# Kernel tuning notes

Measured on AMD Instinct MI355X. Metric: run time of the kernel, lower is better.

The kernel has to match this reference:

```python
import jax, jax.numpy as jnp
import numpy as np

EPS = 1e-6

def _layernorm(x, gamma, beta):
    # normalize over last dim (head_dim)
    mean = x.mean(axis=-1, keepdims=True)
    var = x.var(axis=-1, keepdims=True)
    return gamma * (x - mean) * jax.lax.rsqrt(var + EPS) + beta

def setup_inputs() -> dict:
    key = jax.random.key(0)
    ks = jax.random.split(key, 6)
    B, N, C, H = 2, 2048, 1024, 16
    Dh = C // H
    x = jax.random.normal(ks[0], (B, N, C), dtype=jnp.float32)
    qkv_w = jax.random.normal(ks[1], (C, 3 * C), dtype=jnp.float32) * (1.0 / np.sqrt(C))
    q_gamma = jnp.ones((Dh,), jnp.float32)
    q_beta = jnp.zeros((Dh,), jnp.float32)
    k_gamma = jnp.ones((Dh,), jnp.float32)
    k_beta = jnp.zeros((Dh,), jnp.float32)
    proj_w = jax.random.normal(ks[2], (C, C), dtype=jnp.float32) * (1.0 / np.sqrt(C))
    proj_b = jnp.zeros((C,), jnp.float32)
    return {"x": x, "qkv_w": qkv_w, "q_gamma": q_gamma, "q_beta": q_beta,
            "k_gamma": k_gamma, "k_beta": k_beta, "proj_w": proj_w, "proj_b": proj_b}

def reference(x, qkv_w, q_gamma, q_beta, k_gamma, k_beta, proj_w, proj_b):
    B, N, C = x.shape
    H = 16
    Dh = C // H
    scale = Dh ** -0.5
    qkv = x @ qkv_w                                   # [B,N,3C]
    qkv = qkv.reshape(B, N, 3, H, Dh)
    q = qkv[:, :, 0].transpose(0, 2, 1, 3)            # [B,H,N,Dh]
    k = qkv[:, :, 1].transpose(0, 2, 1, 3)
    v = qkv[:, :, 2].transpose(0, 2, 1, 3)
    q = _layernorm(q, q_gamma, q_beta)
    k = _layernorm(k, k_gamma, k_beta)
    attn = jnp.einsum('bhnd,bhmd->bhnm', q, k) * scale
    attn = jax.nn.softmax(attn, axis=-1)
    out = jnp.einsum('bhnm,bhmd->bhnd', attn, v)      # [B,H,N,Dh]
    out = out.transpose(0, 2, 1, 3).reshape(B, N, C)
    return out @ proj_w + proj_b
```

## Files before the change

### kernel.cpp

```cpp
#include <hip/hip_runtime.h>

typedef unsigned short u16;
typedef unsigned int u32;
typedef float f32x4 __attribute__((ext_vector_type(4)));
typedef float f32x16 __attribute__((ext_vector_type(16)));
typedef short s16x8 __attribute__((ext_vector_type(8)));

#define B_ 2
#define N_ 2048
#define C_ 1024
#define H_ 16
#define BN_ (B_*N_)

#define EXP2F(x) __builtin_amdgcn_exp2f(x)

__device__ __forceinline__ u16 f2bf(float f) {
  union { float f; unsigned u; } c; c.f = f;
  unsigned u = c.u;
  u = (u + 0x7fffu + ((u >> 16) & 1u)) >> 16;
  return (u16)u;
}
__device__ __forceinline__ float bf2f(u16 h) {
  union { unsigned u; float f; } c; c.u = ((unsigned)h) << 16;
  return c.f;
}
__device__ __forceinline__ u32 pack2(float lo, float hi) {
  u32 r;
  asm("v_cvt_pk_bf16_f32 %0, %1, %2" : "=v"(r) : "v"(lo), "v"(hi));
  return r;
}
__device__ __forceinline__ void plswap(u32& a, u32& b) {
  asm volatile("v_permlane32_swap_b32 %0, %1" : "+v"(a), "+v"(b));
}
__device__ __forceinline__ void gload16(const u16* g, u16* l) {
  __builtin_amdgcn_global_load_lds(
      (const __attribute__((address_space(1))) unsigned*)g,
      (__attribute__((address_space(3))) unsigned*)l, 16, 0, 0);
}

__global__ __launch_bounds__(256) void k_cast_bf16(const float* __restrict__ x,
                                                   u16* __restrict__ o, int n4) {
  int i = blockIdx.x * blockDim.x + threadIdx.x;
  if (i >= n4) return;
  float4 v = ((const float4*)x)[i];
  ushort4 r;
  r.x = f2bf(v.x); r.y = f2bf(v.y); r.z = f2bf(v.z); r.w = f2bf(v.w);
  ((ushort4*)o)[i] = r;
}

__global__ __launch_bounds__(256) void k_transpose_cast(const float* __restrict__ W,
                                                        u16* __restrict__ Wt,
                                                        int R, int Cc) {
  __shared__ float t[32][33];
  int tx = threadIdx.x, ty = threadIdx.y;
  int c0 = blockIdx.x * 32, r0 = blockIdx.y * 32;
#pragma unroll
  for (int i = 0; i < 4; ++i)
    t[ty + i * 8][tx] = W[(long)(r0 + ty + i * 8) * Cc + c0 + tx];
  __syncthreads();
#pragma unroll
  for (int i = 0; i < 4; ++i)
    Wt[(long)(c0 + ty + i * 8) * R + r0 + tx] = f2bf(t[tx][ty + i * 8]);
}

__global__ __launch_bounds__(256) void k_gemm_qkv_ln(const u16* __restrict__ A,
                                                     const u16* __restrict__ Bt,
                                                     const float* __restrict__ qg,
                                                     const float* __restrict__ qbeta,
                                                     const float* __restrict__ kg,
                                                     const float* __restrict__ kbeta,
                                                     u16* __restrict__ Qh,
                                                     u16* __restrict__ Kh,
                                                     u16* __restrict__ Vt) {
  const int K = C_;
  __shared__ u16 smem[32768];
  int tid = threadIdx.x;
  int w = tid >> 6, l = tid & 63;
  int l15 = l & 15, lhi = l >> 4;
  int wm = w >> 1, wn = w & 1;
  int rowA = l >> 3;
  int colA = ((l & 7) ^ (rowA & 7)) * 8;
  int x0 = (lhi ^ (l15 & 7)) * 8;
  int x1 = ((4 + lhi) ^ (l15 & 7)) * 8;
  const u16* Ab = A + (long)blockIdx.y * 128 * K;
  const u16* Bb = Bt + (long)blockIdx.x * 128 * K;
  f32x4 acc[4][4];
#pragma unroll
  for (int m = 0; m < 4; ++m)
#pragma unroll
    for (int n = 0; n < 4; ++n)
      acc[m][n] = (f32x4){0.f, 0.f, 0.f, 0.f};

  auto STAGE = [&](int k0, int bi) {
    u16* at = smem + bi * 8192;
    u16* bt = smem + 16384 + bi * 8192;
#pragma unroll
    for (int i = 0; i < 4; ++i) {
      int ci = i * 4 + w;
      gload16(Ab + (long)(ci * 8 + rowA) * K + k0 + colA, &at[ci * 512]);
      gload16(Bb + (long)(ci * 8 + rowA) * K + k0 + colA, &bt[ci * 512]);
    }
  };

  const int NS = K / 64;
  STAGE(0, 0);
  for (int t = 0; t < NS; ++t) {
    __builtin_amdgcn_s_barrier();
    if (t + 1 < NS) {
      STAGE((t + 1) * 64, (t + 1) & 1);
      asm volatile("s_waitcnt vmcnt(8)" ::: "memory");
    } else {
      asm volatile("s_waitcnt vmcnt(0)" ::: "memory");
    }
    __builtin_amdgcn_s_barrier();
    const u16* at = smem + (t & 1) * 8192;
    const u16* bt = smem + 16384 + (t & 1) * 8192;
#pragma unroll
    for (int kk = 0; kk < 2; ++kk) {
      int xo = kk ? x1 : x0;
      s16x8 af[4], bfr[4];
#pragma unroll
      for (int m = 0; m < 4; ++m)
        af[m] = *(const s16x8*)&at[(wm * 64 + m * 16 + l15) * 64 + xo];
#pragma unroll
      for (int n = 0; n < 4; ++n)
        bfr[n] = *(const s16x8*)&bt[(wn * 64 + n * 16 + l15) * 64 + xo];
#pragma unroll
      for (int m = 0; m < 4; ++m)
#pragma unroll
        for (int n = 0; n < 4; ++n)
          acc[m][n] = __builtin_amdgcn_mfma_f32_16x16x32_bf16(af[m], bfr[n], acc[m][n], 0, 0, 0);
    }
  }

  int cb = blockIdx.x * 128 + wn * 64;
  int s = cb >> 10;
  int h = (cb & 1023) >> 6;
  int rowbase = blockIdx.y * 128 + wm * 64;

  if (s == 2) {
    __syncthreads();
    u16* tbuf = smem + w * 4608;
    u32* tb32 = (u32*)tbuf;
#pragma unroll
    for (int m = 0; m < 4; ++m)
#pragma unroll
      for (int n = 0; n < 4; ++n) {
        int d = n * 16 + l15;
#pragma unroll
        for (int r = 0; r < 4; r += 2)
          tb32[d * 36 + m * 8 + lhi * 2 + (r >> 1)] =
              pack2(acc[m][n][r], acc[m][n][r + 1]);
      }
    int b = rowbase >> 11;
    int nnb = rowbase & (N_ - 1);
    int bhv = b * H_ + h;
    int ch = (l & 7) * 8;
#pragma unroll
    for (int i = 0; i < 8; ++i) {
      int dl = i * 8 + (l >> 3);
      s16x8 vv = *(const s16x8*)&tbuf[dl * 72 + ch];
      *(s16x8*)&Vt[(long)(bhv * 64 + dl) * N_ + nnb + ch] = vv;
    }
  } else {
    const float* g = (s == 0) ? qg : kg;
    const float* be = (s == 0) ? qbeta : kbeta;
    u16* Oh = (s == 0) ? Qh : Kh;
    float sc = (s == 0) ? 0.125f * 1.44269504089f : 1.f;
    float gv[4], bv[4];
#pragma unroll
    for (int n = 0; n < 4; ++n) { gv[n] = g[n * 16 + l15]; bv[n] = be[n * 16 + l15]; }
#pragma unroll
    for (int m = 0; m < 4; ++m) {
#pragma unroll
      for (int r = 0; r < 4; ++r) {
        float t = (acc[m][0][r] + acc[m][1][r]) + (acc[m][2][r] + acc[m][3][r]);
        t += __shfl_xor(t, 1); t += __shfl_xor(t, 2);
        t += __shfl_xor(t, 4); t += __shfl_xor(t, 8);
        float mean = t * (1.f / 64.f);
        float v0 = acc[m][0][r] - mean, v1 = acc[m][1][r] - mean;
        float v2 = acc[m][2][r] - mean, v3 = acc[m][3][r] - mean;
        float q2 = (v0 * v0 + v1 * v1) + (v2 * v2 + v3 * v3);
        q2 += __shfl_xor(q2, 1); q2 += __shfl_xor(q2, 2);
        q2 += __shfl_xor(q2, 4); q2 += __shfl_xor(q2, 8);
        float rs = rsqrtf(q2 * (1.f / 64.f) + 1e-6f);
        int row = rowbase + m * 16 + lhi * 4 + r;
        int b = row >> 11, nn = row & (N_ - 1);
        long ob = ((long)(b * H_ + h) * N_ + nn) * 64;
        float vv[4] = {v0, v1, v2, v3};
#pragma unroll
        for (int n = 0; n < 4; ++n)
          Oh[ob + n * 16 + l15] = f2bf(sc * (gv[n] * vv[n] * rs + bv[n]));
      }
    }
  }
}

__global__ __launch_bounds__(256) void k_gemm_proj(const u16* __restrict__ A,
                                                   const u16* __restrict__ Bt,
                                                   float* __restrict__ Cout,
                                                   const float* __restrict__ bias,
                                                   int M, int N, int K) {
  __shared__ u16 a_t[2][128 * 64];
  __shared__ u16 b_t[2][128 * 64];
  int tid = threadIdx.x;
  int w = tid >> 6, l = tid & 63;
  int l15 = l & 15, lhi = l >> 4;
  int wm = w >> 1, wn = w & 1;
  int rowA = l >> 3;
  int colA = ((l & 7) ^ (rowA & 7)) * 8;
  int x0 = (lhi ^ (l15 & 7)) * 8;
  int x1 = ((4 + lhi) ^ (l15 & 7)) * 8;
  const u16* Ab = A + (long)blockIdx.y * 128 * K;
  const u16* Bb = Bt + (long)blockIdx.x * 128 * K;
  f32x4 acc[4][4];
#pragma unroll
  for (int m = 0; m < 4; ++m)
#pragma unroll
    for (int n = 0; n < 4; ++n)
      acc[m][n] = (f32x4){0.f, 0.f, 0.f, 0.f};

  auto STAGE = [&](int k0, int bi) {
#pragma unroll
    for (int i = 0; i < 4; ++i) {
      int ci = i * 4 + w;
      gload16(Ab + (long)(ci * 8 + rowA) * K + k0 + colA, &a_t[bi][ci * 512]);
      gload16(Bb + (long)(ci * 8 + rowA) * K + k0 + colA, &b_t[bi][ci * 512]);
    }
  };

  const int NS = 1024 / 64;
  STAGE(0, 0);
  for (int t = 0; t < NS; ++t) {
    __builtin_amdgcn_s_barrier();
    if (t + 1 < NS) {
      STAGE((t + 1) * 64, (t + 1) & 1);
      asm volatile("s_waitcnt vmcnt(8)" ::: "memory");
    } else {
      asm volatile("s_waitcnt vmcnt(0)" ::: "memory");
    }
    __builtin_amdgcn_s_barrier();
    const u16* at = a_t[t & 1];
    const u16* bt = b_t[t & 1];
#pragma unroll
    for (int kk = 0; kk < 2; ++kk) {
      int xo = kk ? x1 : x0;
      s16x8 af[4], bfr[4];
#pragma unroll
      for (int m = 0; m < 4; ++m)
        af[m] = *(const s16x8*)&at[(wm * 64 + m * 16 + l15) * 64 + xo];
#pragma unroll
      for (int n = 0; n < 4; ++n)
        bfr[n] = *(const s16x8*)&bt[(wn * 64 + n * 16 + l15) * 64 + xo];
#pragma unroll
      for (int m = 0; m < 4; ++m)
#pragma unroll
        for (int n = 0; n < 4; ++n)
          acc[m][n] = __builtin_amdgcn_mfma_f32_16x16x32_bf16(af[m], bfr[n], acc[m][n], 0, 0, 0);
    }
  }
#pragma unroll
  for (int m = 0; m < 4; ++m) {
#pragma unroll
    for (int n = 0; n < 4; ++n) {
      int col = blockIdx.x * 128 + wn * 64 + n * 16 + l15;
#pragma unroll
      for (int r = 0; r < 4; ++r) {
        int row = blockIdx.y * 128 + wm * 64 + m * 16 + lhi * 4 + r;
        Cout[(long)row * N + col] = acc[m][n][r] + bias[col];
      }
    }
  }
}

__global__ __launch_bounds__(512, 4) void k_attn(const u16* __restrict__ Qh,
                                                 const u16* __restrict__ Kh,
                                                 const u16* __restrict__ Vt,
                                                 u16* __restrict__ O) {
  __shared__ u16 k_t[2][2][64 * 64];
  __shared__ u16 v_t[2][2][64 * 64];
  int tid = threadIdx.x;
  int w = tid >> 6, l = tid & 63;
  int half = w >> 2, wq = w & 3;
  int l31 = l & 31, hi = l >> 5;
  int id = blockIdx.x;
  int swz = (id & 7) * 64 + (id >> 3);
  int bh = swz >> 4, qb = swz & 15;
  int b = bh >> 4, h = bh & 15;
  const u16* Qb = Qh + ((long)bh * N_ + qb * 128 + wq * 32) * 64;
  const u16* Kb = Kh + ((long)bh * N_ + half * 1024) * 64;
  const u16* Vb = Vt + (long)bh * 64 * N_ + half * 1024;

  s16x8 qf[4];
#pragma unroll
  for (int j = 0; j < 4; ++j)
    qf[j] = *(const s16x8*)&Qb[l31 * 64 + j * 16 + hi * 8];

  f32x16 acc0, acc1;
#pragma unroll
  for (int i = 0; i < 16; ++i) { acc0[i] = 0.f; acc1[i] = 0.f; }
  float lsum = 0.f;

  int off[2][4];
#pragma unroll
  for (int t = 0; t < 2; ++t)
#pragma unroll
    for (int j = 0; j < 4; ++j)
      off[t][j] = (t * 32 + l31) * 64 + (((j * 2 + hi) ^ (l & 7)) * 8);

  int srow = l >> 3;
  int scol = ((l & 7) ^ srow) * 8;

  auto STAGE = [&](int kt, int bi) {
#pragma unroll
    for (int i = 0; i < 2; ++i) {
      int ci = i * 4 + wq;
      gload16(Kb + (long)(kt + ci * 8 + srow) * 64 + scol, &k_t[half][bi][ci * 512]);
      gload16(Vb + (long)(ci * 8 + srow) * N_ + kt + scol, &v_t[half][bi][ci * 512]);
    }
  };

  const int NT = 16;
  STAGE(0, 0);

  for (int t = 0; t < NT; ++t) {
    __builtin_amdgcn_s_barrier();
    if (t + 1 < NT) {
      STAGE((t + 1) * 64, (t + 1) & 1);
      asm volatile("s_waitcnt vmcnt(4)" ::: "memory");
    } else {
      asm volatile("s_waitcnt vmcnt(0)" ::: "memory");
    }
    __builtin_amdgcn_s_barrier();
    const u16* kb = k_t[half][t & 1];
    const u16* vb = v_t[half][t & 1];

    f32x16 s0, s1;
#pragma unroll
    for (int i = 0; i < 16; ++i) { s0[i] = 0.f; s1[i] = 0.f; }
    __builtin_amdgcn_s_setprio(1);
#pragma unroll
    for (int j = 0; j < 4; ++j) {
      s16x8 kf0 = *(const s16x8*)&kb[off[0][j]];
      s0 = __builtin_amdgcn_mfma_f32_32x32x16_bf16(kf0, qf[j], s0, 0, 0, 0);
      s16x8 kf1 = *(const s16x8*)&kb[off[1][j]];
      s1 = __builtin_amdgcn_mfma_f32_32x32x16_bf16(kf1, qf[j], s1, 0, 0, 0);
    }
    __builtin_amdgcn_s_setprio(0);

#pragma unroll
    for (int i = 0; i < 16; ++i) {
      s0[i] = EXP2F(s0[i]);
      s1[i] = EXP2F(s1[i]);
    }
    f32x16 sm;
#pragma unroll
    for (int i = 0; i < 16; ++i) sm[i] = s0[i] + s1[i];
#pragma unroll
    for (int i = 0; i < 8; ++i) sm[i] += sm[i + 8];
#pragma unroll
    for (int i = 0; i < 4; ++i) sm[i] += sm[i + 4];
    lsum += (sm[0] + sm[1]) + (sm[2] + sm[3]);

    s16x8 pa[4];
#pragma unroll
    for (int g = 0; g < 4; ++g) {
      const f32x16& sv = (g < 2) ? s0 : s1;
      int o = (g & 1) * 8;
      u32 a = pack2(sv[o + 0], sv[o + 1]);
      u32 bb = pack2(sv[o + 4], sv[o + 5]);
      u32 c = pack2(sv[o + 2], sv[o + 3]);
      u32 d = pack2(sv[o + 6], sv[o + 7]);
      plswap(a, bb);
      plswap(c, d);
      union { u32 u[4]; s16x8 v; } fr;
      fr.u[0] = a; fr.u[1] = c; fr.u[2] = bb; fr.u[3] = d;
      pa[g] = fr.v;
    }

    __builtin_amdgcn_s_setprio(1);
#pragma unroll
    for (int j = 0; j < 4; ++j) {
      s16x8 vf0 = *(const s16x8*)&vb[off[0][j]];
      acc0 = __builtin_amdgcn_mfma_f32_32x32x16_bf16(pa[j], vf0, acc0, 0, 0, 0);
      s16x8 vf1 = *(const s16x8*)&vb[off[1][j]];
      acc1 = __builtin_amdgcn_mfma_f32_32x32x16_bf16(pa[j], vf1, acc1, 0, 0, 0);
    }
    __builtin_amdgcn_s_setprio(0);
  }

  lsum += __shfl_xor(lsum, 32);

  __syncthreads();
  float* mbuf = (float*)&k_t[0][0][0];
  float* ml   = (float*)&v_t[0][0][0];

  if (half == 1) {
    if (hi == 0) ml[wq * 32 + l31] = lsum;
#pragma unroll
    for (int r = 0; r < 16; ++r) {
      mbuf[((wq * 32 + r) * 64) + l] = acc0[r];
      mbuf[((wq * 32 + 16 + r) * 64) + l] = acc1[r];
    }
  }
  __syncthreads();

  if (half == 0) {
    float s_b = ml[wq * 32 + l31];
    float lstar = lsum + s_b;
    int lsi = __float_as_int(lstar);
#pragma unroll
    for (int r = 0; r < 16; ++r) {
      int ql = (r & 3) + 8 * (r >> 2) + 4 * hi;
      float ls = __int_as_float(__builtin_amdgcn_ds_bpermute(ql << 2, lsi));
      float o0 = acc0[r] + mbuf[((wq * 32 + r) * 64) + l];
      float o1 = acc1[r] + mbuf[((wq * 32 + 16 + r) * 64) + l];
      float inv = 1.f / ls;
      int q = qb * 128 + wq * 32 + ql;
      long ob = ((long)(b * N_ + q) * H_ + h) * 64 + l31;
      O[ob] = f2bf(o0 * inv);
      O[ob + 32] = f2bf(o1 * inv);
    }
  }
}

extern "C" void kernel_launch(void* const* d_in, const int* in_sizes, int n_in,
                              void* d_out, int out_size, void* d_ws, size_t ws_size,
                              hipStream_t stream) {
  const float* x      = (const float*)d_in[0];
  const float* qkv_w  = (const float*)d_in[1];
  const float* q_g    = (const float*)d_in[2];
  const float* q_b    = (const float*)d_in[3];
  const float* k_g    = (const float*)d_in[4];
  const float* k_b    = (const float*)d_in[5];
  const float* proj_w = (const float*)d_in[6];
  const float* proj_b = (const float*)d_in[7];
  float* out = (float*)d_out;

  char* ws = (char*)d_ws;
  u16* xb     = (u16*)(ws + 0);
  u16* wqkvT  = (u16*)(ws + 8388608);
  u16* wprojT = (u16*)(ws + 14680064);
  u16* Qh     = (u16*)(ws + 16777216);
  u16* Kh     = (u16*)(ws + 25165824);
  u16* Vt     = (u16*)(ws + 41943040);
  u16* attnO  = xb;

  k_cast_bf16<<<4096, 256, 0, stream>>>(x, xb, (BN_ * C_) / 4);
  k_transpose_cast<<<dim3(96, 32), dim3(32, 8), 0, stream>>>(qkv_w, wqkvT, C_, 3 * C_);
  k_transpose_cast<<<dim3(32, 32), dim3(32, 8), 0, stream>>>(proj_w, wprojT, C_, C_);
  k_gemm_qkv_ln<<<dim3(24, 32), 256, 0, stream>>>(xb, wqkvT, q_g, q_b, k_g, k_b, Qh, Kh, Vt);
  k_attn<<<512, 512, 0, stream>>>(Qh, Kh, Vt, attnO);
  k_gemm_proj<<<dim3(8, 32), 256, 0, stream>>>(attnO, wprojT, out, proj_b, BN_, C_, C_);
}
```

Measured before the change: 125.6 us.

## Merge prep kernels into one launch and halve QKV GEMM K-tile

The fp32-to-bf16 cast of x and the two weight transpose-casts now run as a single kernel whose block index picks the job. This removes two kernel launches and the gaps between them. The QKV GEMM now stages 32-wide K slices instead of 64, with a new LDS swizzle and smaller shared memory (sized to the epilogue transpose buffer). That should allow more resident blocks per CU, at the cost of twice as many barrier and wait steps per K pass.

```diff
diff --git a/kernel.cpp b/kernel.cpp
--- a/kernel.cpp
+++ b/kernel.cpp
@@ -38,22 +38,35 @@
       (__attribute__((address_space(3))) unsigned*)l, 16, 0, 0);
 }
 
-__global__ __launch_bounds__(256) void k_cast_bf16(const float* __restrict__ x,
-                                                   u16* __restrict__ o, int n4) {
-  int i = blockIdx.x * blockDim.x + threadIdx.x;
-  if (i >= n4) return;
-  float4 v = ((const float4*)x)[i];
-  ushort4 r;
-  r.x = f2bf(v.x); r.y = f2bf(v.y); r.z = f2bf(v.z); r.w = f2bf(v.w);
-  ((ushort4*)o)[i] = r;
-}
-
-__global__ __launch_bounds__(256) void k_transpose_cast(const float* __restrict__ W,
-                                                        u16* __restrict__ Wt,
-                                                        int R, int Cc) {
+__global__ __launch_bounds__(256) void k_prep(const float* __restrict__ x,
+                                              u16* __restrict__ xb,
+                                              const float* __restrict__ qkv_w,
+                                              u16* __restrict__ wqkvT,
+                                              const float* __restrict__ proj_w,
+                                              u16* __restrict__ wprojT) {
   __shared__ float t[32][33];
-  int tx = threadIdx.x, ty = threadIdx.y;
-  int c0 = blockIdx.x * 32, r0 = blockIdx.y * 32;
+  int bid = blockIdx.x;
+  int tid = threadIdx.x;
+  if (bid < 4096) {
+    int i = bid * 256 + tid;
+    float4 v = ((const float4*)x)[i];
+    ushort4 r;
+    r.x = f2bf(v.x); r.y = f2bf(v.y); r.z = f2bf(v.z); r.w = f2bf(v.w);
+    ((ushort4*)xb)[i] = r;
+    return;
+  }
+  const float* W; u16* Wt; int R, Cc, bx, by;
+  if (bid < 7168) {
+    int b = bid - 4096;
+    bx = b % 96; by = b / 96;
+    W = qkv_w; Wt = wqkvT; R = C_; Cc = 3 * C_;
+  } else {
+    int b = bid - 7168;
+    bx = b & 31; by = b >> 5;
+    W = proj_w; Wt = wprojT; R = C_; Cc = C_;
+  }
+  int tx = tid & 31, ty = tid >> 5;
+  int c0 = bx * 32, r0 = by * 32;
 #pragma unroll
   for (int i = 0; i < 4; ++i)
     t[ty + i * 8][tx] = W[(long)(r0 + ty + i * 8) * Cc + c0 + tx];
@@ -73,15 +86,14 @@
                                                      u16* __restrict__ Kh,
                                                      u16* __restrict__ Vt) {
   const int K = C_;
-  __shared__ u16 smem[32768];
+  __shared__ u16 smem[18432];
   int tid = threadIdx.x;
   int w = tid >> 6, l = tid & 63;
   int l15 = l & 15, lhi = l >> 4;
   int wm = w >> 1, wn = w & 1;
-  int rowA = l >> 3;
-  int colA = ((l & 7) ^ (rowA & 7)) * 8;
-  int x0 = (lhi ^ (l15 & 7)) * 8;
-  int x1 = ((4 + lhi) ^ (l15 & 7)) * 8;
+  int srow = l >> 2;
+  int scol = ((l & 3) ^ ((l >> 3) & 3)) * 8;
+  int xo = (lhi ^ ((l15 >> 1) & 3)) * 8;
   const u16* Ab = A + (long)blockIdx.y * 128 * K;
   const u16* Bb = Bt + (long)blockIdx.x * 128 * K;
   f32x4 acc[4][4];
@@ -92,45 +104,41 @@
       acc[m][n] = (f32x4){0.f, 0.f, 0.f, 0.f};
 
   auto STAGE = [&](int k0, int bi) {
-    u16* at = smem + bi * 8192;
-    u16* bt = smem + 16384 + bi * 8192;
-#pragma unroll
-    for (int i = 0; i < 4; ++i) {
-      int ci = i * 4 + w;
-      gload16(Ab + (long)(ci * 8 + rowA) * K + k0 + colA, &at[ci * 512]);
-      gload16(Bb + (long)(ci * 8 + rowA) * K + k0 + colA, &bt[ci * 512]);
+    u16* at = smem + bi * 4096;
+    u16* bt = smem + 8192 + bi * 4096;
+#pragma unroll
+    for (int i = 0; i < 2; ++i) {
+      int ri = (i * 4 + w) * 16;
+      gload16(Ab + (long)(ri + srow) * K + k0 + scol, &at[ri * 32]);
+      gload16(Bb + (long)(ri + srow) * K + k0 + scol, &bt[ri * 32]);
     }
   };
 
-  const int NS = K / 64;
+  const int NS = K / 32;
   STAGE(0, 0);
   for (int t = 0; t < NS; ++t) {
     __builtin_amdgcn_s_barrier();
     if (t + 1 < NS) {
-      STAGE((t + 1) * 64, (t + 1) & 1);
-      asm volatile("s_waitcnt vmcnt(8)" ::: "memory");
+      STAGE((t + 1) * 32, (t + 1) & 1);
+      asm volatile("s_waitcnt vmcnt(4)" ::: "memory");
     } else {
       asm volatile("s_waitcnt vmcnt(0)" ::: "memory");
     }
     __builtin_amdgcn_s_barrier();
-    const u16* at = smem + (t & 1) * 8192;
-    const u16* bt = smem + 16384 + (t & 1) * 8192;
-#pragma unroll
-    for (int kk = 0; kk < 2; ++kk) {
-      int xo = kk ? x1 : x0;
-      s16x8 af[4], bfr[4];
-#pragma unroll
-      for (int m = 0; m < 4; ++m)
-        af[m] = *(const s16x8*)&at[(wm * 64 + m * 16 + l15) * 64 + xo];
+    const u16* at = smem + (t & 1) * 4096;
+    const u16* bt = smem + 8192 + (t & 1) * 4096;
+    s16x8 af[4], bfr[4];
+#pragma unroll
+    for (int m = 0; m < 4; ++m)
+      af[m] = *(const s16x8*)&at[(wm * 64 + m * 16 + l15) * 32 + xo];
+#pragma unroll
+    for (int n = 0; n < 4; ++n)
+      bfr[n] = *(const s16x8*)&bt[(wn * 64 + n * 16 + l15) * 32 + xo];
+#pragma unroll
+    for (int m = 0; m < 4; ++m)
 #pragma unroll
       for (int n = 0; n < 4; ++n)
-        bfr[n] = *(const s16x8*)&bt[(wn * 64 + n * 16 + l15) * 64 + xo];
-#pragma unroll
-      for (int m = 0; m < 4; ++m)
-#pragma unroll
-        for (int n = 0; n < 4; ++n)
-          acc[m][n] = __builtin_amdgcn_mfma_f32_16x16x32_bf16(af[m], bfr[n], acc[m][n], 0, 0, 0);
-    }
+        acc[m][n] = __builtin_amdgcn_mfma_f32_16x16x32_bf16(af[m], bfr[n], acc[m][n], 0, 0, 0);
   }
 
   int cb = blockIdx.x * 128 + wn * 64;
@@ -446,9 +454,7 @@
   u16* Vt     = (u16*)(ws + 41943040);
   u16* attnO  = xb;
 
-  k_cast_bf16<<<4096, 256, 0, stream>>>(x, xb, (BN_ * C_) / 4);
-  k_transpose_cast<<<dim3(96, 32), dim3(32, 8), 0, stream>>>(qkv_w, wqkvT, C_, 3 * C_);
-  k_transpose_cast<<<dim3(32, 32), dim3(32, 8), 0, stream>>>(proj_w, wprojT, C_, C_);
+  k_prep<<<8192, 256, 0, stream>>>(x, xb, qkv_w, wqkvT, proj_w, wprojT);
   k_gemm_qkv_ln<<<dim3(24, 32), 256, 0, stream>>>(xb, wqkvT, q_g, q_b, k_g, k_b, Qh, Kh, Vt);
   k_attn<<<512, 512, 0, stream>>>(Qh, Kh, Vt, attnO);
   k_gemm_proj<<<dim3(8, 32), 256, 0, stream>>>(attnO, wprojT, out, proj_b, BN_, C_, C_);
```

New measurement: 122.0 us. 2.9% less time.
